# Kernel tuning notes

Hardware: AMD Instinct MI355X
Metric: run time of the kernel (lower is better)

The kernel has to match this reference:

```python
import jax, jax.numpy as jnp
import numpy as np

N_NODES = 50000
N_EDGES = 800000
N_GRAPHS = 256
NEG_SLOPE = 0.2

def selu(x):
    return jax.nn.selu(x)

def gat_conv(x, src, dst, W, att_l, att_r, b, n_nodes):
    """PyG GATConv, heads=1, with self-loops already appended to (src, dst).
    Message j->i: alpha_ij = softmax_i(leaky_relu(a_l.h_j + a_r.h_i)); out_i = sum_j alpha_ij h_j + b."""
    h = x @ W                                   # [N, C]
    a_src = h @ att_l                           # [N]
    a_dst = h @ att_r                           # [N]
    e = jax.nn.leaky_relu(a_src[src] + a_dst[dst], NEG_SLOPE)   # [E]
    # segment softmax over incoming edges of each dst node
    m = jax.ops.segment_max(e, dst, num_segments=n_nodes)       # [N]
    m = jnp.where(jnp.isfinite(m), m, 0.0)
    ex = jnp.exp(e - m[dst])
    denom = jax.ops.segment_sum(ex, dst, num_segments=n_nodes)  # [N]
    alpha = ex / jnp.maximum(denom, 1e-16)[dst]                  # [E]
    out = jax.ops.segment_sum(h[src] * alpha[:, None], dst, num_segments=n_nodes)
    return out + b

def global_mean_pool(x, batch, n_graphs):
    s = jax.ops.segment_sum(x, batch, num_segments=n_graphs)
    cnt = jax.ops.segment_sum(jnp.ones((x.shape[0],), x.dtype), batch, num_segments=n_graphs)
    return s / jnp.maximum(cnt, 1.0)[:, None]

def setup_inputs() -> dict:
    key = jax.random.key(0)
    ks = jax.random.split(key, 12)
    F_in, C, H, NC = 310, 256, 128, 2
    x = jax.random.normal(ks[0], (N_NODES, F_in), dtype=jnp.float32)
    edge_index = jax.random.randint(ks[1], (2, N_EDGES), 0, N_NODES, dtype=jnp.int64)
    batch = jnp.sort(jax.random.randint(ks[2], (N_NODES,), 0, N_GRAPHS, dtype=jnp.int64))
    g = lambda k, shp: jax.random.normal(k, shp, dtype=jnp.float32) * 0.05
    return {
        "x": x, "edge_index": edge_index, "batch": batch,
        "W1": g(ks[3], (F_in, C)), "att_l1": g(ks[4], (C,)), "att_r1": g(ks[5], (C,)),
        "b1": jnp.zeros((C,), jnp.float32),
        "W2": g(ks[6], (C, C)), "att_l2": g(ks[7], (C,)), "att_r2": g(ks[8], (C,)),
        "b2": jnp.zeros((C,), jnp.float32),
        "fc1_W": g(ks[9], (C, H)), "fc1_b": jnp.zeros((H,), jnp.float32),
        "fc2_W": g(ks[10], (H, NC)), "fc2_b": jnp.zeros((NC,), jnp.float32),
    }

def reference(x, edge_index, batch, W1, att_l1, att_r1, b1, W2, att_l2, att_r2, b2,
              fc1_W, fc1_b, fc2_W, fc2_b):
    n = x.shape[0]
    loops = jnp.arange(n, dtype=edge_index.dtype)
    src = jnp.concatenate([edge_index[0], loops])   # add_self_loops=True (PyG default)
    dst = jnp.concatenate([edge_index[1], loops])
    h = selu(gat_conv(x, src, dst, W1, att_l1, att_r1, b1, n))
    h = selu(gat_conv(h, src, dst, W2, att_l2, att_r2, b2, n))
    g = selu(global_mean_pool(h, batch, N_GRAPHS))      # [G, 256]
    g = selu(g @ fc1_W + fc1_b)                         # [G, 128]
    # dropout is identity in eval mode
    return jax.nn.log_softmax(g @ fc2_W + fc2_b, axis=-1)  # [G, 2]
```

## Files before the change

kernel.cpp:

```cpp
#include <hip/hip_runtime.h>
#include <hip/hip_bf16.h>

#define N_NODES 50000
#define N_EDGES 800000
#define N_TOT   (N_EDGES + N_NODES)
#define N_GRAPHS 256
#define F_IN 310
#define KP1 320
#define CH 256
#define HID 128
#define DEG_CAP 128

typedef __attribute__((ext_vector_type(8))) short short8;
typedef __attribute__((ext_vector_type(4))) float f32x4;
typedef unsigned short ushort_t;

__device__ __forceinline__ float selu_f(float x) {
    const float scale = 1.0507009873554805f;
    const float alpha = 1.6732632423543772f;
    return x > 0.f ? scale * x : scale * alpha * (expm1f(x));
}

__device__ __forceinline__ ushort_t f32_to_bf16_rne(float f) {
    unsigned u = __float_as_uint(f);
    unsigned rounding = 0x7FFFu + ((u >> 16) & 1u);
    return (ushort_t)((u + rounding) >> 16);
}
__device__ __forceinline__ float bf16_to_f32(ushort_t v) {
    return __uint_as_float(((unsigned)v) << 16);
}

__global__ __launch_bounds__(256) void convert_pad_x(
        const float* __restrict__ x, ushort_t* __restrict__ A) {
    int i = blockIdx.x * 256 + threadIdx.x;
    if (i >= N_NODES * (KP1 / 2)) return;
    int r = i / (KP1 / 2);
    int c2 = i - r * (KP1 / 2);
    int c = c2 * 2;
    ushort2 o = {0, 0};
    if (c2 < F_IN / 2) {
        float2 v = *(const float2*)(x + (long)r * F_IN + c);
        o.x = f32_to_bf16_rne(v.x);
        o.y = f32_to_bf16_rne(v.y);
    }
    *(ushort2*)(A + (long)r * KP1 + c) = o;
}

__global__ __launch_bounds__(256) void convert_wt(
        const float* __restrict__ W, ushort_t* __restrict__ Wt, int K, int Kp) {
    int i = blockIdx.x * blockDim.x + threadIdx.x;
    if (i >= CH * Kp) return;
    int n = i / Kp, k = i % Kp;
    Wt[i] = (k < K) ? f32_to_bf16_rne(W[(long)k * CH + n]) : 0;
}

__global__ __launch_bounds__(512) void gemm_bf16_fused(
        const ushort_t* __restrict__ A, const ushort_t* __restrict__ Bt,
        ushort_t* __restrict__ Cb, const float* __restrict__ att_l,
        const float* __restrict__ att_r, float* __restrict__ a_src,
        float* __restrict__ a_dst, int M, int Kp) {
    __shared__ __align__(16) ushort_t As[2][128 * 32];
    __shared__ __align__(16) ushort_t Bs[2][256 * 32];
    __shared__ float s_pl[128], s_pr[128];
    int tid = threadIdx.x;
    int row0 = blockIdx.x * 128;
    int w = tid >> 6, l = tid & 63;
    int lr = l & 15, lc = l >> 4;
    int wr = w >> 2, wc = w & 3;
    f32x4 acc[4][4] = {};

    int srow = l >> 2;
    int schunk = l & 3;
    int trowA = w * 16 + srow;
    int sx = schunk ^ (srow & 3);
    int garow = row0 + trowA; if (garow >= M) garow = M - 1;
    const ushort_t* gA  = A  + (size_t)garow * Kp + sx * 8;
    const ushort_t* gB0 = Bt + (size_t)trowA * Kp + sx * 8;
    const ushort_t* gB1 = Bt + (size_t)(128 + trowA) * Kp + sx * 8;
    int nt = Kp >> 5;

    auto stage = [&](int sel, int k0) {
        __builtin_amdgcn_global_load_lds(
            (const __attribute__((address_space(1))) void*)(gA + k0),
            (__attribute__((address_space(3))) void*)(&As[sel][w * 16 * 32]), 16, 0, 0);
        __builtin_amdgcn_global_load_lds(
            (const __attribute__((address_space(1))) void*)(gB0 + k0),
            (__attribute__((address_space(3))) void*)(&Bs[sel][w * 16 * 32]), 16, 0, 0);
        __builtin_amdgcn_global_load_lds(
            (const __attribute__((address_space(1))) void*)(gB1 + k0),
            (__attribute__((address_space(3))) void*)(&Bs[sel][(128 + w * 16) * 32]), 16, 0, 0);
    };

    stage(0, 0);
    __syncthreads();
    int cur = 0;
    for (int t = 0; t < nt; ++t) {
        if (t + 1 < nt) stage(cur ^ 1, (t + 1) << 5);
        short8 af[4], bf[4];
#pragma unroll
        for (int mi = 0; mi < 4; ++mi) {
            int r = wr * 64 + mi * 16 + lr;
            af[mi] = *(const short8*)(&As[cur][r * 32 + ((lc ^ (r & 3)) * 8)]);
        }
#pragma unroll
        for (int ni = 0; ni < 4; ++ni) {
            int r = wc * 64 + ni * 16 + lr;
            bf[ni] = *(const short8*)(&Bs[cur][r * 32 + ((lc ^ (r & 3)) * 8)]);
        }
#pragma unroll
        for (int mi = 0; mi < 4; ++mi)
#pragma unroll
            for (int ni = 0; ni < 4; ++ni)
                acc[mi][ni] = __builtin_amdgcn_mfma_f32_16x16x32_bf16(
                    af[mi], bf[ni], acc[mi][ni], 0, 0, 0);
        __syncthreads();
        cur ^= 1;
    }

    if (tid < 128) { s_pl[tid] = 0.f; s_pr[tid] = 0.f; }
    __syncthreads();
    float al[4], ar[4];
#pragma unroll
    for (int ni = 0; ni < 4; ++ni) {
        int col = wc * 64 + ni * 16 + lr;
        al[ni] = att_l[col];
        ar[ni] = att_r[col];
    }
#pragma unroll
    for (int mi = 0; mi < 4; ++mi) {
        int lrow = wr * 64 + mi * 16 + lc * 4;
#pragma unroll
        for (int q = 0; q < 4; ++q) {
            int grow = row0 + lrow + q;
            float pl = 0.f, pr = 0.f;
#pragma unroll
            for (int ni = 0; ni < 4; ++ni) {
                float v = acc[mi][ni][q];
                pl += v * al[ni];
                pr += v * ar[ni];
                if (grow < M)
                    Cb[(size_t)grow * CH + wc * 64 + ni * 16 + lr] = f32_to_bf16_rne(v);
            }
#pragma unroll
            for (int off = 1; off < 16; off <<= 1) {
                pl += __shfl_xor(pl, off);
                pr += __shfl_xor(pr, off);
            }
            if (lr == 0) {
                atomicAdd(&s_pl[lrow + q], pl);
                atomicAdd(&s_pr[lrow + q], pr);
            }
        }
    }
    __syncthreads();
    if (tid < 128 && row0 + tid < M) {
        a_src[row0 + tid] = s_pl[tid];
        a_dst[row0 + tid] = s_pr[tid];
    }
}

__global__ __launch_bounds__(256) void deg_count(
        const int* __restrict__ ei, int* __restrict__ deg) {
    int eid = blockIdx.x * blockDim.x + threadIdx.x;
    if (eid >= N_TOT) return;
    int d = (eid < N_EDGES) ? ei[N_EDGES + eid] : eid - N_EDGES;
    atomicAdd(&deg[d], 1);
}

__global__ __launch_bounds__(256) void reserve_k(
        const int* __restrict__ deg, int* __restrict__ start,
        int* __restrict__ fillpos, int* __restrict__ cursor, int n) {
    int i = blockIdx.x * blockDim.x + threadIdx.x;
    if (i >= n) return;
    int s = atomicAdd(cursor, deg[i]);
    start[i] = s;
    fillpos[i] = s;
}

__global__ __launch_bounds__(256) void csr_fill(
        const int* __restrict__ ei, int* __restrict__ fillpos,
        int* __restrict__ csr_src) {
    int eid = blockIdx.x * blockDim.x + threadIdx.x;
    if (eid >= N_TOT) return;
    int s, d;
    if (eid < N_EDGES) { s = ei[eid]; d = ei[N_EDGES + eid]; }
    else { s = eid - N_EDGES; d = s; }
    int p = atomicAdd(&fillpos[d], 1);
    csr_src[p] = s;
}

__global__ __launch_bounds__(256) void gat_aggregate(
        const int* __restrict__ start, const int* __restrict__ deg,
        const int* __restrict__ csr_src,
        const float* __restrict__ a_src, const float* __restrict__ a_dst,
        const ushort_t* __restrict__ h, const float* __restrict__ bias,
        ushort_t* __restrict__ out_bf, int n) {
    __shared__ int   s_idx[4][DEG_CAP];
    __shared__ float s_ex[4][DEG_CAP];
    int wid = threadIdx.x >> 6;
    int lane = threadIdx.x & 63;
    int node = blockIdx.x * 4 + wid;
    if (node >= n) return;
    int s0 = start[node];
    int dg = deg[node];
    float ad = a_dst[node];
    bool cached = (dg <= DEG_CAP);

    float sum = 0.f;
    for (int i = lane; i < dg; i += 64) {
        int s = csr_src[s0 + i];
        float e = a_src[s] + ad;
        e = fmaxf(e, 0.2f * e);
        float ex = __expf(e);
        if (cached) { s_idx[wid][i] = s; s_ex[wid][i] = ex; }
        sum += ex;
    }
#pragma unroll
    for (int off = 32; off > 0; off >>= 1) sum += __shfl_xor(sum, off);
    float inv = 1.f / fmaxf(sum, 1e-16f);

    float4 acc = {0.f, 0.f, 0.f, 0.f};
    if (cached) {
        int i = 0;
        for (; i + 4 <= dg; i += 4) {
            int sa = s_idx[wid][i],     sb = s_idx[wid][i + 1];
            int sc_ = s_idx[wid][i + 2], sd = s_idx[wid][i + 3];
            float xa = s_ex[wid][i] * inv,     xb = s_ex[wid][i + 1] * inv;
            float xc = s_ex[wid][i + 2] * inv, xd = s_ex[wid][i + 3] * inv;
            ushort4 ha = *(const ushort4*)(h + (long)sa * CH + lane * 4);
            ushort4 hb = *(const ushort4*)(h + (long)sb * CH + lane * 4);
            ushort4 hc = *(const ushort4*)(h + (long)sc_ * CH + lane * 4);
            ushort4 hd = *(const ushort4*)(h + (long)sd * CH + lane * 4);
            acc.x += xa * bf16_to_f32(ha.x) + xb * bf16_to_f32(hb.x)
                   + xc * bf16_to_f32(hc.x) + xd * bf16_to_f32(hd.x);
            acc.y += xa * bf16_to_f32(ha.y) + xb * bf16_to_f32(hb.y)
                   + xc * bf16_to_f32(hc.y) + xd * bf16_to_f32(hd.y);
            acc.z += xa * bf16_to_f32(ha.z) + xb * bf16_to_f32(hb.z)
                   + xc * bf16_to_f32(hc.z) + xd * bf16_to_f32(hd.z);
            acc.w += xa * bf16_to_f32(ha.w) + xb * bf16_to_f32(hb.w)
                   + xc * bf16_to_f32(hc.w) + xd * bf16_to_f32(hd.w);
        }
        for (; i < dg; i++) {
            int s = s_idx[wid][i];
            float xa = s_ex[wid][i] * inv;
            ushort4 hv = *(const ushort4*)(h + (long)s * CH + lane * 4);
            acc.x += xa * bf16_to_f32(hv.x);
            acc.y += xa * bf16_to_f32(hv.y);
            acc.z += xa * bf16_to_f32(hv.z);
            acc.w += xa * bf16_to_f32(hv.w);
        }
    } else {
        for (int i = 0; i < dg; i++) {
            int s = csr_src[s0 + i];
            float e = a_src[s] + ad;
            e = fmaxf(e, 0.2f * e);
            float alpha = __expf(e) * inv;
            ushort4 hv = *(const ushort4*)(h + (long)s * CH + lane * 4);
            acc.x += alpha * bf16_to_f32(hv.x);
            acc.y += alpha * bf16_to_f32(hv.y);
            acc.z += alpha * bf16_to_f32(hv.z);
            acc.w += alpha * bf16_to_f32(hv.w);
        }
    }
    float4 bv = *(const float4*)(bias + lane * 4);
    ushort4 ob;
    ob.x = f32_to_bf16_rne(selu_f(acc.x + bv.x));
    ob.y = f32_to_bf16_rne(selu_f(acc.y + bv.y));
    ob.z = f32_to_bf16_rne(selu_f(acc.z + bv.z));
    ob.w = f32_to_bf16_rne(selu_f(acc.w + bv.w));
    *(ushort4*)(out_bf + (long)node * CH + lane * 4) = ob;
}

__global__ __launch_bounds__(256) void pool_kernel(
        const ushort_t* __restrict__ h, const int* __restrict__ batch,
        float* __restrict__ g1) {
    int g = blockIdx.x;
    int t = threadIdx.x;
    int lo, hi;
    { int a = 0, b = N_NODES;
      while (a < b) { int mid = (a + b) >> 1; if (batch[mid] < g) a = mid + 1; else b = mid; }
      lo = a; }
    { int a = lo, b = N_NODES;
      while (a < b) { int mid = (a + b) >> 1; if (batch[mid] < g + 1) a = mid + 1; else b = mid; }
      hi = a; }
    float a0 = 0.f, a1 = 0.f, a2 = 0.f, a3 = 0.f;
    int i = lo;
    for (; i + 3 < hi; i += 4) {
        a0 += bf16_to_f32(h[(long)i * CH + t]);
        a1 += bf16_to_f32(h[(long)(i + 1) * CH + t]);
        a2 += bf16_to_f32(h[(long)(i + 2) * CH + t]);
        a3 += bf16_to_f32(h[(long)(i + 3) * CH + t]);
    }
    for (; i < hi; i++) a0 += bf16_to_f32(h[(long)i * CH + t]);
    float acc = (a0 + a1) + (a2 + a3);
    float cnt = (float)(hi - lo);
    g1[g * CH + t] = selu_f(acc / fmaxf(cnt, 1.f));
}

__global__ __launch_bounds__(128) void head_kernel(
        const float* __restrict__ g1, const float* __restrict__ fc1W,
        const float* __restrict__ fc1b, const float* __restrict__ fc2W,
        const float* __restrict__ fc2b, float* __restrict__ out) {
    __shared__ float row[CH];
    __shared__ float hrow[HID];
    __shared__ float logits[2];
    int g = blockIdx.x, t = threadIdx.x;
    row[t] = g1[g * CH + t];
    row[t + 128] = g1[g * CH + t + 128];
    __syncthreads();
    float acc = fc1b[t];
    for (int k = 0; k < CH; k++) acc += row[k] * fc1W[k * HID + t];
    hrow[t] = selu_f(acc);
    __syncthreads();
    if (t < 2) {
        float a = fc2b[t];
        for (int k = 0; k < HID; k++) a += hrow[k] * fc2W[k * 2 + t];
        logits[t] = a;
    }
    __syncthreads();
    if (t < 2) {
        float m = fmaxf(logits[0], logits[1]);
        float lse = logf(expf(logits[0] - m) + expf(logits[1] - m)) + m;
        out[g * 2 + t] = logits[t] - lse;
    }
}

extern "C" void kernel_launch(void* const* d_in, const int* in_sizes, int n_in,
                              void* d_out, int out_size, void* d_ws, size_t ws_size,
                              hipStream_t stream) {
    const float* x      = (const float*)d_in[0];
    const int*   ei     = (const int*)d_in[1];
    const int*   batch  = (const int*)d_in[2];
    const float* W1     = (const float*)d_in[3];
    const float* att_l1 = (const float*)d_in[4];
    const float* att_r1 = (const float*)d_in[5];
    const float* b1     = (const float*)d_in[6];
    const float* W2     = (const float*)d_in[7];
    const float* att_l2 = (const float*)d_in[8];
    const float* att_r2 = (const float*)d_in[9];
    const float* b2     = (const float*)d_in[10];
    const float* fc1W   = (const float*)d_in[11];
    const float* fc1b   = (const float*)d_in[12];
    const float* fc2W   = (const float*)d_in[13];
    const float* fc2b   = (const float*)d_in[14];
    float* out = (float*)d_out;

    char* ws = (char*)d_ws;
    size_t off = 0;
    auto alloc = [&](size_t bytes) {
        void* p = ws + off;
        off += (bytes + 255) & ~(size_t)255;
        return p;
    };
    ushort_t* Ab     = (ushort_t*)alloc((size_t)N_NODES * KP1 * 2);
    ushort_t* Hb1    = (ushort_t*)alloc((size_t)N_NODES * CH * 2);
    ushort_t* Zb2    = (ushort_t*)alloc((size_t)N_NODES * CH * 2);
    ushort_t* Hb2    = (ushort_t*)alloc((size_t)N_NODES * CH * 2);
    ushort_t* W1t    = (ushort_t*)alloc((size_t)CH * KP1 * 2);
    ushort_t* W2t    = (ushort_t*)alloc((size_t)CH * CH * 2);
    float*    a_src  = (float*)alloc((size_t)N_NODES * 4);
    float*    a_dst  = (float*)alloc((size_t)N_NODES * 4);
    int*      deg    = (int*)alloc((size_t)N_NODES * 4);
    int*      startA = (int*)alloc((size_t)N_NODES * 4);
    int*      fillpos= (int*)alloc((size_t)N_NODES * 4);
    int*      csr_src= (int*)alloc((size_t)N_TOT * 4);
    int*      cursor = (int*)alloc(256);
    float*    g1     = (float*)alloc((size_t)N_GRAPHS * CH * 4);

    dim3 blk(256);
    int gemm_grid = (N_NODES + 127) / 128;
    int conv_grid = (N_NODES * (KP1 / 2) + 255) / 256;
    int edge_grid = (N_TOT + 255) / 256;
    int node_grid = (N_NODES + 255) / 256;
    int agg_grid  = (N_NODES + 3) / 4;

    convert_pad_x<<<conv_grid, blk, 0, stream>>>(x, Ab);
    convert_wt<<<(CH * KP1 + 255) / 256, blk, 0, stream>>>(W1, W1t, F_IN, KP1);
    convert_wt<<<(CH * CH + 255) / 256, blk, 0, stream>>>(W2, W2t, CH, CH);
    hipMemsetAsync(deg, 0, (size_t)N_NODES * 4, stream);
    hipMemsetAsync(cursor, 0, 4, stream);
    deg_count<<<edge_grid, blk, 0, stream>>>(ei, deg);
    reserve_k<<<node_grid, blk, 0, stream>>>(deg, startA, fillpos, cursor, N_NODES);
    csr_fill<<<edge_grid, blk, 0, stream>>>(ei, fillpos, csr_src);

    gemm_bf16_fused<<<gemm_grid, dim3(512), 0, stream>>>(Ab, W1t, Hb1, att_l1, att_r1,
                                                         a_src, a_dst, N_NODES, KP1);
    gat_aggregate<<<agg_grid, blk, 0, stream>>>(startA, deg, csr_src, a_src, a_dst,
                                                Hb1, b1, Zb2, N_NODES);

    gemm_bf16_fused<<<gemm_grid, dim3(512), 0, stream>>>(Zb2, W2t, Hb2, att_l2, att_r2,
                                                         a_src, a_dst, N_NODES, CH);
    gat_aggregate<<<agg_grid, blk, 0, stream>>>(startA, deg, csr_src, a_src, a_dst,
                                                Hb2, b2, Hb1, N_NODES);

    pool_kernel<<<N_GRAPHS, blk, 0, stream>>>(Hb1, batch, g1);
    head_kernel<<<N_GRAPHS, dim3(128), 0, stream>>>(g1, fc1W, fc1b, fc2W, fc2b, out);
}
```

Baseline: 329.9 us.

## Merge weight converts, fuse pool+head, retile GEMM to 64 rows, unroll gather by 8

Merges the two weight-conversion kernels into one launch and fuses the pooling and MLP head kernels, which removes the g1 intermediate. The two memsets are folded into one by placing cursor right after deg. The GEMM changes from 128x256 tiles with 512 threads to 64x256 tiles with 256 threads, so it launches more blocks. The aggregation inner loop gets an 8-way unrolled gather to keep more loads in flight. These aim to cut launch overhead and raise memory-level parallelism, at the cost of reloading B more often per row in the GEMM and more register pressure in the gather.

```diff
diff --git a/kernel.cpp b/kernel.cpp
--- a/kernel.cpp
+++ b/kernel.cpp
@@ -46,49 +46,55 @@
     *(ushort2*)(A + (long)r * KP1 + c) = o;
 }
 
-__global__ __launch_bounds__(256) void convert_wt(
-        const float* __restrict__ W, ushort_t* __restrict__ Wt, int K, int Kp) {
+__global__ __launch_bounds__(256) void convert_wt_both(
+        const float* __restrict__ W1, ushort_t* __restrict__ W1t,
+        const float* __restrict__ W2, ushort_t* __restrict__ W2t) {
     int i = blockIdx.x * blockDim.x + threadIdx.x;
-    if (i >= CH * Kp) return;
-    int n = i / Kp, k = i % Kp;
-    Wt[i] = (k < K) ? f32_to_bf16_rne(W[(long)k * CH + n]) : 0;
-}
-
-__global__ __launch_bounds__(512) void gemm_bf16_fused(
+    const int n1 = CH * KP1;
+    if (i < n1) {
+        int n = i / KP1, k = i % KP1;
+        W1t[i] = (k < F_IN) ? f32_to_bf16_rne(W1[(long)k * CH + n]) : 0;
+    } else {
+        int j = i - n1;
+        if (j >= CH * CH) return;
+        int n = j / CH, k = j % CH;
+        W2t[j] = f32_to_bf16_rne(W2[(long)k * CH + n]);
+    }
+}
+
+__global__ __launch_bounds__(256) void gemm_bf16_fused(
         const ushort_t* __restrict__ A, const ushort_t* __restrict__ Bt,
         ushort_t* __restrict__ Cb, const float* __restrict__ att_l,
         const float* __restrict__ att_r, float* __restrict__ a_src,
         float* __restrict__ a_dst, int M, int Kp) {
-    __shared__ __align__(16) ushort_t As[2][128 * 32];
+    __shared__ __align__(16) ushort_t As[2][64 * 32];
     __shared__ __align__(16) ushort_t Bs[2][256 * 32];
-    __shared__ float s_pl[128], s_pr[128];
+    __shared__ float s_pl[64], s_pr[64];
     int tid = threadIdx.x;
-    int row0 = blockIdx.x * 128;
+    int row0 = blockIdx.x * 64;
     int w = tid >> 6, l = tid & 63;
     int lr = l & 15, lc = l >> 4;
-    int wr = w >> 2, wc = w & 3;
     f32x4 acc[4][4] = {};
 
     int srow = l >> 2;
-    int schunk = l & 3;
-    int trowA = w * 16 + srow;
-    int sx = schunk ^ (srow & 3);
-    int garow = row0 + trowA; if (garow >= M) garow = M - 1;
-    const ushort_t* gA  = A  + (size_t)garow * Kp + sx * 8;
-    const ushort_t* gB0 = Bt + (size_t)trowA * Kp + sx * 8;
-    const ushort_t* gB1 = Bt + (size_t)(128 + trowA) * Kp + sx * 8;
+    int sx = (l & 3) ^ (srow & 3);
+    int garow = row0 + w * 16 + srow; if (garow >= M) garow = M - 1;
+    const ushort_t* gA = A + (size_t)garow * Kp + sx * 8;
+    const ushort_t* gB[4];
+#pragma unroll
+    for (int g = 0; g < 4; ++g)
+        gB[g] = Bt + (size_t)(w * 64 + g * 16 + srow) * Kp + sx * 8;
     int nt = Kp >> 5;
 
     auto stage = [&](int sel, int k0) {
         __builtin_amdgcn_global_load_lds(
             (const __attribute__((address_space(1))) void*)(gA + k0),
             (__attribute__((address_space(3))) void*)(&As[sel][w * 16 * 32]), 16, 0, 0);
-        __builtin_amdgcn_global_load_lds(
-            (const __attribute__((address_space(1))) void*)(gB0 + k0),
-            (__attribute__((address_space(3))) void*)(&Bs[sel][w * 16 * 32]), 16, 0, 0);
-        __builtin_amdgcn_global_load_lds(
-            (const __attribute__((address_space(1))) void*)(gB1 + k0),
-            (__attribute__((address_space(3))) void*)(&Bs[sel][(128 + w * 16) * 32]), 16, 0, 0);
+#pragma unroll
+        for (int g = 0; g < 4; ++g)
+            __builtin_amdgcn_global_load_lds(
+                (const __attribute__((address_space(1))) void*)(gB[g] + k0),
+                (__attribute__((address_space(3))) void*)(&Bs[sel][(w * 64 + g * 16) * 32]), 16, 0, 0);
     };
 
     stage(0, 0);
@@ -99,12 +105,12 @@
         short8 af[4], bf[4];
 #pragma unroll
         for (int mi = 0; mi < 4; ++mi) {
-            int r = wr * 64 + mi * 16 + lr;
+            int r = mi * 16 + lr;
             af[mi] = *(const short8*)(&As[cur][r * 32 + ((lc ^ (r & 3)) * 8)]);
         }
 #pragma unroll
         for (int ni = 0; ni < 4; ++ni) {
-            int r = wc * 64 + ni * 16 + lr;
+            int r = w * 64 + ni * 16 + lr;
             bf[ni] = *(const short8*)(&Bs[cur][r * 32 + ((lc ^ (r & 3)) * 8)]);
         }
 #pragma unroll
@@ -117,18 +123,18 @@
         cur ^= 1;
     }
 
-    if (tid < 128) { s_pl[tid] = 0.f; s_pr[tid] = 0.f; }
+    if (tid < 64) { s_pl[tid] = 0.f; s_pr[tid] = 0.f; }
     __syncthreads();
     float al[4], ar[4];
 #pragma unroll
     for (int ni = 0; ni < 4; ++ni) {
-        int col = wc * 64 + ni * 16 + lr;
+        int col = w * 64 + ni * 16 + lr;
         al[ni] = att_l[col];
         ar[ni] = att_r[col];
     }
 #pragma unroll
     for (int mi = 0; mi < 4; ++mi) {
-        int lrow = wr * 64 + mi * 16 + lc * 4;
+        int lrow = mi * 16 + lc * 4;
 #pragma unroll
         for (int q = 0; q < 4; ++q) {
             int grow = row0 + lrow + q;
@@ -139,7 +145,7 @@
                 pl += v * al[ni];
                 pr += v * ar[ni];
                 if (grow < M)
-                    Cb[(size_t)grow * CH + wc * 64 + ni * 16 + lr] = f32_to_bf16_rne(v);
+                    Cb[(size_t)grow * CH + w * 64 + ni * 16 + lr] = f32_to_bf16_rne(v);
             }
 #pragma unroll
             for (int off = 1; off < 16; off <<= 1) {
@@ -153,7 +159,7 @@
         }
     }
     __syncthreads();
-    if (tid < 128 && row0 + tid < M) {
+    if (tid < 64 && row0 + tid < M) {
         a_src[row0 + tid] = s_pl[tid];
         a_dst[row0 + tid] = s_pr[tid];
     }
@@ -222,6 +228,26 @@
     float4 acc = {0.f, 0.f, 0.f, 0.f};
     if (cached) {
         int i = 0;
+        for (; i + 8 <= dg; i += 8) {
+            int   si[8];
+            float xi[8];
+            ushort4 hv[8];
+#pragma unroll
+            for (int j = 0; j < 8; ++j) {
+                si[j] = s_idx[wid][i + j];
+                xi[j] = s_ex[wid][i + j] * inv;
+            }
+#pragma unroll
+            for (int j = 0; j < 8; ++j)
+                hv[j] = *(const ushort4*)(h + (long)si[j] * CH + lane * 4);
+#pragma unroll
+            for (int j = 0; j < 8; ++j) {
+                acc.x += xi[j] * bf16_to_f32(hv[j].x);
+                acc.y += xi[j] * bf16_to_f32(hv[j].y);
+                acc.z += xi[j] * bf16_to_f32(hv[j].z);
+                acc.w += xi[j] * bf16_to_f32(hv[j].w);
+            }
+        }
         for (; i + 4 <= dg; i += 4) {
             int sa = s_idx[wid][i],     sb = s_idx[wid][i + 1];
             int sc_ = s_idx[wid][i + 2], sd = s_idx[wid][i + 3];
@@ -271,9 +297,14 @@
     *(ushort4*)(out_bf + (long)node * CH + lane * 4) = ob;
 }
 
-__global__ __launch_bounds__(256) void pool_kernel(
+__global__ __launch_bounds__(256) void pool_head_kernel(
         const ushort_t* __restrict__ h, const int* __restrict__ batch,
-        float* __restrict__ g1) {
+        const float* __restrict__ fc1W, const float* __restrict__ fc1b,
+        const float* __restrict__ fc2W, const float* __restrict__ fc2b,
+        float* __restrict__ out) {
+    __shared__ float row[CH];
+    __shared__ float hrow[HID];
+    __shared__ float logits[2];
     int g = blockIdx.x;
     int t = threadIdx.x;
     int lo, hi;
@@ -294,23 +325,13 @@
     for (; i < hi; i++) a0 += bf16_to_f32(h[(long)i * CH + t]);
     float acc = (a0 + a1) + (a2 + a3);
     float cnt = (float)(hi - lo);
-    g1[g * CH + t] = selu_f(acc / fmaxf(cnt, 1.f));
-}
-
-__global__ __launch_bounds__(128) void head_kernel(
-        const float* __restrict__ g1, const float* __restrict__ fc1W,
-        const float* __restrict__ fc1b, const float* __restrict__ fc2W,
-        const float* __restrict__ fc2b, float* __restrict__ out) {
-    __shared__ float row[CH];
-    __shared__ float hrow[HID];
-    __shared__ float logits[2];
-    int g = blockIdx.x, t = threadIdx.x;
-    row[t] = g1[g * CH + t];
-    row[t + 128] = g1[g * CH + t + 128];
-    __syncthreads();
-    float acc = fc1b[t];
-    for (int k = 0; k < CH; k++) acc += row[k] * fc1W[k * HID + t];
-    hrow[t] = selu_f(acc);
+    row[t] = selu_f(acc / fmaxf(cnt, 1.f));
+    __syncthreads();
+    if (t < HID) {
+        float s = fc1b[t];
+        for (int k = 0; k < CH; k++) s += row[k] * fc1W[k * HID + t];
+        hrow[t] = selu_f(s);
+    }
     __syncthreads();
     if (t < 2) {
         float a = fc2b[t];
@@ -361,38 +382,38 @@
     float*    a_src  = (float*)alloc((size_t)N_NODES * 4);
     float*    a_dst  = (float*)alloc((size_t)N_NODES * 4);
     int*      deg    = (int*)alloc((size_t)N_NODES * 4);
+    int*      cursor = (int*)alloc(256);
     int*      startA = (int*)alloc((size_t)N_NODES * 4);
     int*      fillpos= (int*)alloc((size_t)N_NODES * 4);
     int*      csr_src= (int*)alloc((size_t)N_TOT * 4);
-    int*      cursor = (int*)alloc(256);
-    float*    g1     = (float*)alloc((size_t)N_GRAPHS * CH * 4);
+
+    size_t deg_pad = ((size_t)N_NODES * 4 + 255) & ~(size_t)255;
 
     dim3 blk(256);
-    int gemm_grid = (N_NODES + 127) / 128;
+    int gemm_grid = (N_NODES + 63) / 64;
     int conv_grid = (N_NODES * (KP1 / 2) + 255) / 256;
+    int wt_grid   = (CH * KP1 + CH * CH + 255) / 256;
     int edge_grid = (N_TOT + 255) / 256;
     int node_grid = (N_NODES + 255) / 256;
     int agg_grid  = (N_NODES + 3) / 4;
 
     convert_pad_x<<<conv_grid, blk, 0, stream>>>(x, Ab);
-    convert_wt<<<(CH * KP1 + 255) / 256, blk, 0, stream>>>(W1, W1t, F_IN, KP1);
-    convert_wt<<<(CH * CH + 255) / 256, blk, 0, stream>>>(W2, W2t, CH, CH);
-    hipMemsetAsync(deg, 0, (size_t)N_NODES * 4, stream);
-    hipMemsetAsync(cursor, 0, 4, stream);
+    convert_wt_both<<<wt_grid, blk, 0, stream>>>(W1, W1t, W2, W2t);
+    hipMemsetAsync(deg, 0, deg_pad + 4, stream);
     deg_count<<<edge_grid, blk, 0, stream>>>(ei, deg);
     reserve_k<<<node_grid, blk, 0, stream>>>(deg, startA, fillpos, cursor, N_NODES);
     csr_fill<<<edge_grid, blk, 0, stream>>>(ei, fillpos, csr_src);
 
-    gemm_bf16_fused<<<gemm_grid, dim3(512), 0, stream>>>(Ab, W1t, Hb1, att_l1, att_r1,
-                                                         a_src, a_dst, N_NODES, KP1);
+    gemm_bf16_fused<<<gemm_grid, blk, 0, stream>>>(Ab, W1t, Hb1, att_l1, att_r1,
+                                                   a_src, a_dst, N_NODES, KP1);
     gat_aggregate<<<agg_grid, blk, 0, stream>>>(startA, deg, csr_src, a_src, a_dst,
                                                 Hb1, b1, Zb2, N_NODES);
 
-    gemm_bf16_fused<<<gemm_grid, dim3(512), 0, stream>>>(Zb2, W2t, Hb2, att_l2, att_r2,
-                                                         a_src, a_dst, N_NODES, CH);
+    gemm_bf16_fused<<<gemm_grid, blk, 0, stream>>>(Zb2, W2t, Hb2, att_l2, att_r2,
+                                                   a_src, a_dst, N_NODES, CH);
     gat_aggregate<<<agg_grid, blk, 0, stream>>>(startA, deg, csr_src, a_src, a_dst,
                                                 Hb2, b2, Hb1, N_NODES);
 
-    pool_kernel<<<N_GRAPHS, blk, 0, stream>>>(Hb1, batch, g1);
-    head_kernel<<<N_GRAPHS, dim3(128), 0, stream>>>(g1, fc1W, fc1b, fc2W, fc2b, out);
-}
+    pool_head_kernel<<<N_GRAPHS, blk, 0, stream>>>(Hb1, batch, fc1W, fc1b,
+                                                   fc2W, fc2b, out);
+}
```

After: 333.0 us. Within noise of the previous version (+1.0%).
